# Kernel optimization log

Measured on AMD Instinct MI355X. Metric: run time of the kernel, lower is better.

## Reference

```python
import jax, jax.numpy as jnp
import numpy as np

INPUT_DIM = 512
HEAD_NUM = 8
ATT_SIZE = 64
EPS = 1e-5


def layer_norm(x, g, b):
    mu = jnp.mean(x, axis=-1, keepdims=True)
    var = jnp.mean(jnp.square(x - mu), axis=-1, keepdims=True)
    return (x - mu) * jax.lax.rsqrt(var + EPS) * g + b


def setup_inputs() -> dict:
    key = jax.random.key(0)
    ks = jax.random.split(key, 10)
    D, H, A = INPUT_DIM, HEAD_NUM, ATT_SIZE
    HA = H * A
    s = lambda fan_in: 1.0 / np.sqrt(fan_in)
    x = jax.random.normal(ks[0], (32, 6, 256, D), dtype=jnp.float32)
    # Linear weights stored as [in, out] so y = x @ W + b (matches torch x @ W.T)
    Wq = jax.random.uniform(ks[1], (D, HA), jnp.float32, -s(D), s(D))
    bq = jnp.zeros((HA,), jnp.float32)
    Wk = jax.random.uniform(ks[2], (D, HA), jnp.float32, -s(D), s(D))
    bk = jnp.zeros((HA,), jnp.float32)
    Wv = jax.random.uniform(ks[3], (D, HA), jnp.float32, -s(D), s(D))
    bv = jnp.zeros((HA,), jnp.float32)
    Wo = jax.random.uniform(ks[4], (HA, D), jnp.float32, -s(HA), s(HA))
    bo = jnp.zeros((D,), jnp.float32)
    g1 = jnp.ones((D,), jnp.float32)
    b1 = jnp.zeros((D,), jnp.float32)
    Wd = jax.random.uniform(ks[5], (2 * D, D), jnp.float32, -s(2 * D), s(2 * D))
    bd = jnp.zeros((D,), jnp.float32)
    g2 = jnp.ones((D,), jnp.float32)
    b2 = jnp.zeros((D,), jnp.float32)
    return dict(x=x, Wq=Wq, bq=bq, Wk=Wk, bk=bk, Wv=Wv, bv=bv,
                Wo=Wo, bo=bo, g1=g1, b1=b1, Wd=Wd, bd=bd, g2=g2, b2=b2)


def reference(x, Wq, bq, Wk, bk, Wv, bv, Wo, bo, g1, b1, Wd, bd, g2, b2):
    B, M, P, D = x.shape
    H, A = HEAD_NUM, ATT_SIZE
    # QKV projections -> [B, M, H, P, A]
    q = (x @ Wq + bq).reshape(B, M, P, H, A).transpose(0, 1, 3, 2, 4)
    k = (x @ Wk + bk).reshape(B, M, P, H, A).transpose(0, 1, 3, 2, 4)
    v = (x @ Wv + bv).reshape(B, M, P, H, A).transpose(0, 1, 3, 2, 4)
    scores = jnp.einsum('bmhqa,bmhka->bmhqk', q, k) / jnp.sqrt(jnp.float32(A))
    attn = jax.nn.softmax(scores, axis=-1)
    z = jnp.einsum('bmhqk,bmhka->bmhqa', attn, v)
    z = z.transpose(0, 1, 3, 2, 4).reshape(B, M, P, H * A)
    z = jax.nn.relu(x + layer_norm(z @ Wo + bo, g1, b1))
    # patch merge (1/2 downsample)
    if P % 2:  # static shape check, fine under jit
        z = jnp.pad(z, ((0, 0), (0, 0), (0, 1), (0, 0)))
    merged = jnp.concatenate([z[:, :, 0::2, :], z[:, :, 1::2, :]], axis=-1)
    out = jax.nn.relu(layer_norm(merged @ Wd + bd, g2, b2))
    return out
```

## Files before the change

kernel.cpp:

```cpp
#include <hip/hip_runtime.h>
#include <hip/hip_bf16.h>
#include <stdint.h>


typedef __hip_bfloat16 bf16;
typedef __attribute__((ext_vector_type(8))) __bf16 bf16v8;
typedef __attribute__((ext_vector_type(4))) float f32x4;
typedef __attribute__((ext_vector_type(8))) short s16x8;
typedef __attribute__((ext_vector_type(4))) short s16x4;

static __device__ __forceinline__ void gl_lds16(const void* src, void* dst) {
  __builtin_amdgcn_global_load_lds((const __attribute__((address_space(1))) void*)src,
                                   (__attribute__((address_space(3))) void*)dst,
                                   16, 0, 0);
}

static __device__ __forceinline__ unsigned short f2bfu(float f) {
  return __builtin_bit_cast(unsigned short, __float2bfloat16(f));
}
static __device__ __forceinline__ float bfu2f(unsigned short u) {
  return __builtin_bit_cast(float, (unsigned int)u << 16);
}

__global__ __launch_bounds__(256) void conv_x_kernel(const float4* __restrict__ x,
                                                     s16x4* __restrict__ xb, int n4) {
  int stride = gridDim.x * 256;
  for (int i = blockIdx.x * 256 + threadIdx.x; i < n4; i += stride) {
    float4 v = x[i];
    s16x4 o;
    o[0] = (short)f2bfu(v.x); o[1] = (short)f2bfu(v.y);
    o[2] = (short)f2bfu(v.z); o[3] = (short)f2bfu(v.w);
    xb[i] = o;
  }
}

__global__ __launch_bounds__(256) void conv_w_kernel(
    const float* __restrict__ Wq, const float* __restrict__ Wk, const float* __restrict__ Wv,
    const float* __restrict__ Wo, const float* __restrict__ Wd,
    const float* __restrict__ bq, const float* __restrict__ bk, const float* __restrict__ bv,
    bf16* __restrict__ wqkv_t, bf16* __restrict__ wo_t, bf16* __restrict__ wd_t,
    float* __restrict__ bqkv) {
  int o = blockIdx.x * 256 + threadIdx.x;
  if (o < 786432) {
    int j = o >> 9, kk = o & 511;
    const float* W = (j < 512) ? Wq : (j < 1024) ? Wk : Wv;
    wqkv_t[o] = __float2bfloat16(W[kk * 512 + (j & 511)]);
  } else if (o < 1048576) {
    int o2 = o - 786432; int j = o2 >> 9, kk = o2 & 511;
    wo_t[o2] = __float2bfloat16(Wo[kk * 512 + j]);
  } else if (o < 1572864) {
    int o3 = o - 1048576; int j = o3 >> 10, kk = o3 & 1023;
    wd_t[o3] = __float2bfloat16(Wd[kk * 512 + j]);
  } else if (o < 1574400) {
    int o4 = o - 1572864;
    const float* b = (o4 < 512) ? bq : (o4 < 1024) ? bk : bv;
    bqkv[o4] = b[o4 & 511];
  }
}

template<int EPI, int AMODE>
__global__ __launch_bounds__(512, 2) void gemm256(
    const bf16* __restrict__ A, const bf16* __restrict__ Bt,
    const float* __restrict__ bias, int K,
    bf16* __restrict__ oq, bf16* __restrict__ ok, bf16* __restrict__ ovt,
    bf16* __restrict__ obf) {
  __shared__ __align__(16) char smem[131072];
  const int tid = threadIdx.x;
  const int wave = tid >> 6, lane = tid & 63;
  const int wr = wave >> 2, wc = wave & 3;
  const int lane15 = lane & 15, g = lane >> 4;
  const int tileM = blockIdx.x * 256, tileN = blockIdx.y * 256;

  const int rT = tid >> 3;
  const int cT = (tid & 7) ^ (rT & 7);

  const int iters = K >> 7;

  auto stage = [&](int tau, int q) {
    char* dst = smem + ((tau & 1) << 16) + ((q >> 1) << 15) + ((q & 1) << 14) + tid * 16;
    int kpos = tau * 64 + cT * 8;
    if (q < 2) {
      int rowA = tileM + ((q & 1) << 7) + rT;
      if (AMODE == 0) {
        const bf16* s0 = A + (size_t)rowA * K + kpos;
        gl_lds16(s0, dst);
        gl_lds16(s0 + (size_t)64 * K, dst + 8192);
      } else {
#pragma unroll
        for (int j = 0; j < 2; ++j) {
          int mr = rowA + j * 64;
          int bm = mr >> 7, pp = mr & 127;
          const bf16* s = A + (size_t)(bm * 256 + pp * 2 + (kpos >> 9)) * 512 + (kpos & 511);
          gl_lds16(s, dst + j * 8192);
        }
      }
    } else {
      int rowB = tileN + ((q & 1) << 7) + rT;
      const bf16* s0 = Bt + (size_t)rowB * K + kpos;
      gl_lds16(s0, dst);
      gl_lds16(s0 + (size_t)64 * K, dst + 8192);
    }
  };

  f32x4 acc[8][4] = {};
  bf16v8 areg[4][2], breg[2][2];

  stage(0, 0); stage(0, 1); stage(0, 2); stage(0, 3);
  stage(1, 0); stage(1, 1);
  asm volatile("s_waitcnt vmcnt(4)" ::: "memory");
  __builtin_amdgcn_s_barrier();

  for (int it = 0; it < iters; ++it) {
    const bool last = (it == iters - 1);
#pragma unroll
    for (int p = 0; p < 8; ++p) {
      const int buf = p >> 2;
      const int mh = (p >> 1) & 1, nh = p & 1;
      char* Ab = smem + (buf << 16);
      char* Bb = Ab + 32768;
      if (nh == 0) {
#pragma unroll
        for (int f = 0; f < 4; ++f) {
          int row = wr * 128 + (mh * 4 + f) * 16 + lane15;
#pragma unroll
          for (int ks = 0; ks < 2; ++ks)
            areg[f][ks] = *(const bf16v8*)(Ab + row * 128 + (((ks * 4 + g) ^ (row & 7)) << 4));
        }
      }
#pragma unroll
      for (int n = 0; n < 2; ++n) {
        int row = wc * 64 + (nh * 2 + n) * 16 + lane15;
#pragma unroll
        for (int ks = 0; ks < 2; ++ks)
          breg[n][ks] = *(const bf16v8*)(Bb + row * 128 + (((ks * 4 + g) ^ (row & 7)) << 4));
      }
      if (p == 0)      { stage(2 * it + 1, 2); stage(2 * it + 1, 3); }
      else if (p == 3) { if (!last) { stage(2 * it + 2, 0); stage(2 * it + 2, 1); } }
      else if (p == 4) { if (!last) { stage(2 * it + 2, 2); stage(2 * it + 2, 3); } }
      else if (p == 7) { if (!last) { stage(2 * it + 3, 0); stage(2 * it + 3, 1); } }
      __builtin_amdgcn_s_setprio(1);
#pragma unroll
      for (int ks = 0; ks < 2; ++ks)
#pragma unroll
        for (int f = 0; f < 4; ++f)
#pragma unroll
          for (int n = 0; n < 2; ++n)
            acc[mh * 4 + f][nh * 2 + n] = __builtin_amdgcn_mfma_f32_16x16x32_bf16(
                areg[f][ks], breg[n][ks], acc[mh * 4 + f][nh * 2 + n], 0, 0, 0);
      __builtin_amdgcn_s_setprio(0);
      if (p == 2 || p == 6) {
        asm volatile("s_waitcnt lgkmcnt(0)" ::: "memory");
        __builtin_amdgcn_s_barrier();
      } else if (p == 3) {
        if (last) { asm volatile("s_waitcnt vmcnt(0) lgkmcnt(0)" ::: "memory"); }
        else      { asm volatile("s_waitcnt vmcnt(4) lgkmcnt(0)" ::: "memory"); }
        __builtin_amdgcn_s_barrier();
      } else if (p == 7) {
        if (last) { asm volatile("s_waitcnt lgkmcnt(0)" ::: "memory"); }
        else      { asm volatile("s_waitcnt vmcnt(4) lgkmcnt(0)" ::: "memory"); }
        __builtin_amdgcn_s_barrier();
      }
    }
  }

  if (EPI == 0 && tileN >= 1024) {
    const int hh = ((tileN - 1024) >> 6) + wc;
    const int bm = tileM >> 8;
    char* slab = smem + wave * 16384;
#pragma unroll
    for (int fm = 0; fm < 8; ++fm) {
#pragma unroll
      for (int fn = 0; fn < 4; ++fn) {
        int col = tileN + wc * 64 + fn * 16 + lane15;
        float bb = bias[col];
        int a = fn * 16 + lane15;
#pragma unroll
        for (int i = 0; i < 4; ++i) {
          int pl = fm * 16 + g * 4 + i;
          *(bf16*)(slab + a * 256 + ((pl * 2) ^ ((a & 7) << 4))) =
              __float2bfloat16(acc[fm][fn][i] + bb);
        }
      }
    }
    asm volatile("" ::: "memory");
    bf16* vdst = ovt + ((size_t)(bm * 8 + hh) << 14) + wr * 128;
#pragma unroll
    for (int r = 0; r < 16; ++r) {
      int a = r * 4 + (lane >> 4);
      int ps = lane & 15;
      s16x8 vv = *(const s16x8*)(slab + a * 256 + ((ps * 16) ^ ((a & 7) << 4)));
      *(s16x8*)(vdst + a * 256 + ps * 8) = vv;
    }
  } else {
    char* slab = smem + wave * 16384;
#pragma unroll
    for (int fm = 0; fm < 8; ++fm) {
#pragma unroll
      for (int fn = 0; fn < 4; ++fn) {
        int col = tileN + wc * 64 + fn * 16 + lane15;
        float bb = bias[col];
        int lb = (fn * 16 + lane15) * 2;
#pragma unroll
        for (int i = 0; i < 4; ++i) {
          int pl = fm * 16 + g * 4 + i;
          *(bf16*)(slab + pl * 128 + (lb ^ ((((pl >> 2) & 3)) << 5))) =
              __float2bfloat16(acc[fm][fn][i] + bb);
        }
      }
    }
    asm volatile("" ::: "memory");
    bf16* dst; int ldc2;
    if (EPI == 0) {
      int cb = tileN + wc * 64;
      int hh = (cb >> 6) & 7;
      bf16* base = (cb < 512) ? oq : ok;
      dst = base + (((size_t)((tileM >> 8) * 8 + hh)) << 14) + wr * 128 * 64;
      ldc2 = 64;
    } else {
      dst = obf + (size_t)(tileM + wr * 128) * 512 + tileN + wc * 64;
      ldc2 = 512;
    }
#pragma unroll
    for (int r = 0; r < 16; ++r) {
      int s = r * 64 + lane;
      int pl = s >> 3, sl = s & 7;
      s16x8 vv = *(const s16x8*)(slab + pl * 128 + ((sl * 16) ^ ((((pl >> 2) & 3)) << 5)));
      *(s16x8*)(dst + (size_t)pl * ldc2 + sl * 8) = vv;
    }
  }
}

__global__ __launch_bounds__(256) void attn_kernel(const bf16* __restrict__ q,
                                                   const bf16* __restrict__ k,
                                                   const bf16* __restrict__ vt,
                                                   bf16* __restrict__ z) {
  __shared__ __align__(16) char smem[81920];
  const int tid = threadIdx.x, wave = tid >> 6, lane = tid & 63;
  const int lane15 = lane & 15, g = lane >> 4;
  const int qc = blockIdx.x, hh = blockIdx.y, bm = blockIdx.z;
  const int bh = bm * 8 + hh;
  const bf16* kbase = k + ((size_t)bh << 14);
  const bf16* vbase = vt + ((size_t)bh << 14);
  const bf16* qbase = q + ((size_t)bh << 14) + (qc * 64 + wave * 16) * 64;

#pragma unroll
  for (int i = 0; i < 8; ++i) {
    int s = i * 256 + tid;
    int kr = s >> 3, ksp = s & 7;
    gl_lds16(kbase + kr * 64 + (ksp ^ (kr & 7)) * 8, smem + s * 16);
    int ar = s >> 5, asp = s & 31;
    gl_lds16(vbase + ar * 256 + (asp ^ (ar & 7)) * 8, smem + 32768 + s * 16);
  }
  bf16v8 qf[2];
#pragma unroll
  for (int kk = 0; kk < 2; ++kk)
    qf[kk] = *(const bf16v8*)(qbase + lane15 * 64 + kk * 32 + g * 8);
  __syncthreads();

  f32x4 sacc[16] = {};
#pragma unroll
  for (int tl = 0; tl < 16; ++tl) {
    int key = tl * 16 + lane15;
    int rb = key * 128, swk = (key & 7) << 4;
#pragma unroll
    for (int kk = 0; kk < 2; ++kk) {
      bf16v8 kf = *(const bf16v8*)(smem + rb + (((kk * 4 + g) * 16) ^ swk));
      sacc[tl] = __builtin_amdgcn_mfma_f32_16x16x32_bf16(qf[kk], kf, sacc[tl], 0, 0, 0);
    }
  }

  float mx[4], sm[4], rcp[4];
#pragma unroll
  for (int i = 0; i < 4; ++i) mx[i] = sacc[0][i];
#pragma unroll
  for (int tl = 1; tl < 16; ++tl)
#pragma unroll
    for (int i = 0; i < 4; ++i) mx[i] = fmaxf(mx[i], sacc[tl][i]);
#pragma unroll
  for (int i = 0; i < 4; ++i) {
    mx[i] = fmaxf(mx[i], __shfl_xor(mx[i], 1));
    mx[i] = fmaxf(mx[i], __shfl_xor(mx[i], 2));
    mx[i] = fmaxf(mx[i], __shfl_xor(mx[i], 4));
    mx[i] = fmaxf(mx[i], __shfl_xor(mx[i], 8));
    sm[i] = 0.f;
  }
#pragma unroll
  for (int tl = 0; tl < 16; ++tl)
#pragma unroll
    for (int i = 0; i < 4; ++i) {
      float e = __expf((sacc[tl][i] - mx[i]) * 0.125f);
      sacc[tl][i] = e; sm[i] += e;
    }
#pragma unroll
  for (int i = 0; i < 4; ++i) {
    sm[i] += __shfl_xor(sm[i], 1);
    sm[i] += __shfl_xor(sm[i], 2);
    sm[i] += __shfl_xor(sm[i], 4);
    sm[i] += __shfl_xor(sm[i], 8);
    rcp[i] = 1.0f / sm[i];
  }

  char* pbase = smem + 65536 + wave * 4096;
  f32x4 oacc[4] = {};
#pragma unroll
  for (int h2 = 0; h2 < 2; ++h2) {
#pragma unroll
    for (int t8 = 0; t8 < 8; ++t8) {
      int tl = h2 * 8 + t8;
#pragma unroll
      for (int i = 0; i < 4; ++i) {
        int r = g * 4 + i;
        int c2 = t8 * 16 + lane15;
        *(bf16*)(pbase + r * 256 + ((c2 * 2) ^ ((r & 7) << 4))) =
            __float2bfloat16(sacc[tl][i] * rcp[i]);
      }
    }
    asm volatile("" ::: "memory");
#pragma unroll
    for (int k2 = 0; k2 < 4; ++k2) {
      int ks = h2 * 4 + k2;
      bf16v8 pf = *(const bf16v8*)(pbase + lane15 * 256 +
                                   ((k2 * 64 + g * 16) ^ ((lane15 & 7) << 4)));
#pragma unroll
      for (int at = 0; at < 4; ++at) {
        int a = at * 16 + lane15;
        bf16v8 vf = *(const bf16v8*)(smem + 32768 + a * 512 +
                                     ((ks * 64 + g * 16) ^ ((a & 7) << 4)));
        oacc[at] = __builtin_amdgcn_mfma_f32_16x16x32_bf16(pf, vf, oacc[at], 0, 0, 0);
      }
    }
    asm volatile("" ::: "memory");
  }

  int trow = bm * 256 + qc * 64 + wave * 16;
#pragma unroll
  for (int at = 0; at < 4; ++at)
#pragma unroll
    for (int i = 0; i < 4; ++i)
      z[(size_t)(trow + g * 4 + i) * 512 + hh * 64 + at * 16 + lane15] =
          __float2bfloat16(oacc[at][i]);
}

static __device__ __forceinline__ float wredsum(float v) {
  v += __shfl_xor(v, 1);  v += __shfl_xor(v, 2);  v += __shfl_xor(v, 4);
  v += __shfl_xor(v, 8);  v += __shfl_xor(v, 16); v += __shfl_xor(v, 32);
  return v;
}

__global__ __launch_bounds__(256) void ln_res_kernel(const bf16* __restrict__ y1,
                                                     const float* __restrict__ x,
                                                     const float* __restrict__ g1,
                                                     const float* __restrict__ b1,
                                                     bf16* __restrict__ z2) {
  const int wave = threadIdx.x >> 6, lane = threadIdx.x & 63;
  const int row = blockIdx.x * 4 + wave;
  const size_t base = (size_t)row * 512 + lane * 8;
  s16x8 yv = *(const s16x8*)(y1 + base);
  float f[8];
#pragma unroll
  for (int j = 0; j < 8; ++j) f[j] = bfu2f((unsigned short)yv[j]);
  float s = 0.f, s2 = 0.f;
#pragma unroll
  for (int j = 0; j < 8; ++j) { s += f[j]; s2 += f[j] * f[j]; }
  s = wredsum(s); s2 = wredsum(s2);
  float mu = s * (1.f / 512.f);
  float var = s2 * (1.f / 512.f) - mu * mu;
  float rs = rsqrtf(var + 1e-5f);
  float4 x0 = *(const float4*)(x + base);
  float4 x1 = *(const float4*)(x + base + 4);
  float xa[8] = {x0.x, x0.y, x0.z, x0.w, x1.x, x1.y, x1.z, x1.w};
  float ga[8], ba[8];
#pragma unroll
  for (int j = 0; j < 8; ++j) { ga[j] = g1[lane * 8 + j]; ba[j] = b1[lane * 8 + j]; }
  s16x8 ov;
#pragma unroll
  for (int j = 0; j < 8; ++j) {
    float v = xa[j] + (f[j] - mu) * rs * ga[j] + ba[j];
    ov[j] = (short)f2bfu(fmaxf(v, 0.f));
  }
  *(s16x8*)(z2 + base) = ov;
}

__global__ __launch_bounds__(256) void ln_out_kernel(const bf16* __restrict__ y2,
                                                     const float* __restrict__ g2,
                                                     const float* __restrict__ b2,
                                                     float* __restrict__ out) {
  const int wave = threadIdx.x >> 6, lane = threadIdx.x & 63;
  const int row = blockIdx.x * 4 + wave;
  const size_t base = (size_t)row * 512 + lane * 8;
  s16x8 yv = *(const s16x8*)(y2 + base);
  float f[8];
#pragma unroll
  for (int j = 0; j < 8; ++j) f[j] = bfu2f((unsigned short)yv[j]);
  float s = 0.f, s2 = 0.f;
#pragma unroll
  for (int j = 0; j < 8; ++j) { s += f[j]; s2 += f[j] * f[j]; }
  s = wredsum(s); s2 = wredsum(s2);
  float mu = s * (1.f / 512.f);
  float var = s2 * (1.f / 512.f) - mu * mu;
  float rs = rsqrtf(var + 1e-5f);
  float o[8];
#pragma unroll
  for (int j = 0; j < 8; ++j)
    o[j] = fmaxf((f[j] - mu) * rs * g2[lane * 8 + j] + b2[lane * 8 + j], 0.f);
  float4 w0 = {o[0], o[1], o[2], o[3]};
  float4 w1 = {o[4], o[5], o[6], o[7]};
  *(float4*)(out + base) = w0;
  *(float4*)(out + base + 4) = w1;
}

extern "C" void kernel_launch(void* const* d_in, const int* in_sizes, int n_in,
                              void* d_out, int out_size, void* d_ws, size_t ws_size,
                              hipStream_t stream) {
  const float* x  = (const float*)d_in[0];
  const float* Wq = (const float*)d_in[1];
  const float* bq = (const float*)d_in[2];
  const float* Wk = (const float*)d_in[3];
  const float* bk = (const float*)d_in[4];
  const float* Wv = (const float*)d_in[5];
  const float* bv = (const float*)d_in[6];
  const float* Wo = (const float*)d_in[7];
  const float* bo = (const float*)d_in[8];
  const float* g1 = (const float*)d_in[9];
  const float* b1 = (const float*)d_in[10];
  const float* Wd = (const float*)d_in[11];
  const float* bd = (const float*)d_in[12];
  const float* g2 = (const float*)d_in[13];
  const float* b2 = (const float*)d_in[14];

  char* ws = (char*)d_ws;
  const size_t SEG = 50331648;
  bf16*  xb   = (bf16*)(ws);
  bf16*  qb   = (bf16*)(ws + SEG);
  bf16*  kb   = (bf16*)(ws + 2 * SEG);
  bf16*  vtb  = (bf16*)(ws + 3 * SEG);
  bf16*  wqkv = (bf16*)(ws + 4 * SEG);
  bf16*  wot  = (bf16*)(ws + 4 * SEG + 1572864);
  bf16*  wdt  = (bf16*)(ws + 4 * SEG + 2097152);
  float* bqkv = (float*)(ws + 4 * SEG + 3145728);
  bf16*  zb   = xb;
  bf16*  y1   = qb;
  bf16*  z2   = kb;
  bf16*  y2   = vtb;

  conv_x_kernel<<<4096, 256, 0, stream>>>((const float4*)x, (s16x4*)xb, 25165824 / 4);
  conv_w_kernel<<<6150, 256, 0, stream>>>(Wq, Wk, Wv, Wo, Wd, bq, bk, bv,
                                          wqkv, wot, wdt, bqkv);
  gemm256<0, 0><<<dim3(192, 6), 512, 0, stream>>>(xb, wqkv, bqkv, 512,
                                                  qb, kb, vtb, nullptr);
  attn_kernel<<<dim3(4, 8, 192), 256, 0, stream>>>(qb, kb, vtb, zb);
  gemm256<1, 0><<<dim3(192, 2), 512, 0, stream>>>(zb, wot, bo, 512,
                                                  nullptr, nullptr, nullptr, y1);
  ln_res_kernel<<<12288, 256, 0, stream>>>(y1, x, g1, b1, z2);
  gemm256<1, 1><<<dim3(96, 2), 512, 0, stream>>>(z2, wdt, bd, 1024,
                                                 nullptr, nullptr, nullptr, y2);
  ln_out_kernel<<<6144, 256, 0, stream>>>(y2, g2, b2, (float*)d_out);
}
```

Measured before the change: 337.6 us.

## Restructure GEMM main loop with double-buffered A fragments and per-phase staging

Reworks the 256x256 bf16 GEMM main loop so A fragments are held in two register sets and prefetched one phase ahead of the MFMAs that use them. Global-to-LDS staging is spread as one quarter-tile per phase instead of pairs at fixed phases, with vmcnt waits retuned to match. It also precomputes the swizzled LDS offsets once. Each phase now has two barriers, which adds synchronisation cost and raises register pressure at the 512-thread, 2-block launch bound, in exchange for better overlap of LDS reads with MFMA work.

```diff
diff --git a/kernel.cpp b/kernel.cpp
--- a/kernel.cpp
+++ b/kernel.cpp
@@ -73,8 +73,10 @@
 
   const int rT = tid >> 3;
   const int cT = (tid & 7) ^ (rT & 7);
-
   const int iters = K >> 7;
+
+  const int aoff0 = lane15 * 128 + ((g ^ (lane15 & 7)) << 4);
+  const int aoff1 = lane15 * 128 + (((4 + g) ^ (lane15 & 7)) << 4);
 
   auto stage = [&](int tau, int q) {
     char* dst = smem + ((tau & 1) << 16) + ((q >> 1) << 15) + ((q & 1) << 14) + tid * 16;
@@ -103,41 +105,50 @@
   };
 
   f32x4 acc[8][4] = {};
-  bf16v8 areg[4][2], breg[2][2];
-
-  stage(0, 0); stage(0, 1); stage(0, 2); stage(0, 3);
-  stage(1, 0); stage(1, 1);
-  asm volatile("s_waitcnt vmcnt(4)" ::: "memory");
+  bf16v8 aregA[4][2], aregB[4][2];
+
+#define LOAD_A(SET, BUF, MH)                                                     \
+  {                                                                              \
+    char* a0 = smem + ((BUF) << 16) + aoff0;                                     \
+    char* a1 = smem + ((BUF) << 16) + aoff1;                                     \
+    _Pragma("unroll")                                                            \
+    for (int f = 0; f < 4; ++f) {                                                \
+      SET[f][0] = *(const bf16v8*)(a0 + ((wr * 128 + (MH) * 64 + f * 16) << 7)); \
+      SET[f][1] = *(const bf16v8*)(a1 + ((wr * 128 + (MH) * 64 + f * 16) << 7)); \
+    }                                                                            \
+  }
+
+  stage(0, 0); stage(0, 1); stage(0, 2); stage(0, 3); stage(1, 0);
+  asm volatile("s_waitcnt vmcnt(2)" ::: "memory");
   __builtin_amdgcn_s_barrier();
+  asm volatile("" ::: "memory");
+  LOAD_A(aregA, 0, 0);
 
   for (int it = 0; it < iters; ++it) {
-    const bool last = (it == iters - 1);
 #pragma unroll
     for (int p = 0; p < 8; ++p) {
       const int buf = p >> 2;
       const int mh = (p >> 1) & 1, nh = p & 1;
-      char* Ab = smem + (buf << 16);
-      char* Bb = Ab + 32768;
-      if (nh == 0) {
-#pragma unroll
-        for (int f = 0; f < 4; ++f) {
-          int row = wr * 128 + (mh * 4 + f) * 16 + lane15;
-#pragma unroll
-          for (int ks = 0; ks < 2; ++ks)
-            areg[f][ks] = *(const bf16v8*)(Ab + row * 128 + (((ks * 4 + g) ^ (row & 7)) << 4));
+      bf16v8 breg[2][2];
+      {
+        char* b0 = smem + (buf << 16) + 32768 + aoff0;
+        char* b1 = smem + (buf << 16) + 32768 + aoff1;
+#pragma unroll
+        for (int n = 0; n < 2; ++n) {
+          breg[n][0] = *(const bf16v8*)(b0 + ((wc * 64 + nh * 32 + n * 16) << 7));
+          breg[n][1] = *(const bf16v8*)(b1 + ((wc * 64 + nh * 32 + n * 16) << 7));
         }
       }
-#pragma unroll
-      for (int n = 0; n < 2; ++n) {
-        int row = wc * 64 + (nh * 2 + n) * 16 + lane15;
-#pragma unroll
-        for (int ks = 0; ks < 2; ++ks)
-          breg[n][ks] = *(const bf16v8*)(Bb + row * 128 + (((ks * 4 + g) ^ (row & 7)) << 4));
-      }
-      if (p == 0)      { stage(2 * it + 1, 2); stage(2 * it + 1, 3); }
-      else if (p == 3) { if (!last) { stage(2 * it + 2, 0); stage(2 * it + 2, 1); } }
-      else if (p == 4) { if (!last) { stage(2 * it + 2, 2); stage(2 * it + 2, 3); } }
-      else if (p == 7) { if (!last) { stage(2 * it + 3, 0); stage(2 * it + 3, 1); } }
+      if (p == 1) LOAD_A(aregB, 0, 1);
+      if (p == 3) LOAD_A(aregA, 1, 0);
+      if (p == 5) LOAD_A(aregB, 1, 1);
+      if (p == 7) LOAD_A(aregA, 0, 0);
+      {
+        int idx = it * 8 + p + 5;
+        if (idx < 8 * iters) stage(idx >> 2, idx & 3);
+      }
+      __builtin_amdgcn_s_barrier();
+      asm volatile("" ::: "memory");
       __builtin_amdgcn_s_setprio(1);
 #pragma unroll
       for (int ks = 0; ks < 2; ++ks)
@@ -146,22 +157,21 @@
 #pragma unroll
           for (int n = 0; n < 2; ++n)
             acc[mh * 4 + f][nh * 2 + n] = __builtin_amdgcn_mfma_f32_16x16x32_bf16(
-                areg[f][ks], breg[n][ks], acc[mh * 4 + f][nh * 2 + n], 0, 0, 0);
+                ((p >> 1) & 1) ? aregB[f][ks] : aregA[f][ks], breg[n][ks],
+                acc[mh * 4 + f][nh * 2 + n], 0, 0, 0);
       __builtin_amdgcn_s_setprio(0);
-      if (p == 2 || p == 6) {
-        asm volatile("s_waitcnt lgkmcnt(0)" ::: "memory");
-        __builtin_amdgcn_s_barrier();
-      } else if (p == 3) {
-        if (last) { asm volatile("s_waitcnt vmcnt(0) lgkmcnt(0)" ::: "memory"); }
-        else      { asm volatile("s_waitcnt vmcnt(4) lgkmcnt(0)" ::: "memory"); }
-        __builtin_amdgcn_s_barrier();
-      } else if (p == 7) {
-        if (last) { asm volatile("s_waitcnt lgkmcnt(0)" ::: "memory"); }
-        else      { asm volatile("s_waitcnt vmcnt(4) lgkmcnt(0)" ::: "memory"); }
-        __builtin_amdgcn_s_barrier();
-      }
-    }
-  }
+      const bool lastit = (it == iters - 1);
+      if (p == 2)            { asm volatile("s_waitcnt vmcnt(4)" ::: "memory"); }
+      else if (p == 3) { if (lastit) { asm volatile("s_waitcnt vmcnt(0)" ::: "memory"); }
+                         else        { asm volatile("s_waitcnt vmcnt(2)" ::: "memory"); } }
+      else if (p == 6) { if (lastit) { asm volatile("s_waitcnt vmcnt(0)" ::: "memory"); }
+                         else        { asm volatile("s_waitcnt vmcnt(4)" ::: "memory"); } }
+      else if (p == 7) { if (!lastit) { asm volatile("s_waitcnt vmcnt(2)" ::: "memory"); } }
+      __builtin_amdgcn_s_barrier();
+      asm volatile("" ::: "memory");
+    }
+  }
+#undef LOAD_A
 
   if (EPI == 0 && tileN >= 1024) {
     const int hh = ((tileN - 1024) >> 6) + wc;
```

Measured after the change: 346.5 us. 1.03x slower.
